# Kernel tuning notes

Hardware: AMD Instinct MI355X
Metric: run time of the kernel (lower is better)

## Reference

```python
import jax, jax.numpy as jnp
import numpy as np

N_CLASS = 20
N_SIGMA = 2
H = W = 512
B = 4
N_INST = 32
W_INST, W_VAR, W_SEED = 1.0, 10.0, 1.0
FG_WEIGHT = 10.0


def _xym():
    # channel 0: x along width, channel 1: y along height (matches torch buffer)
    xm = jnp.broadcast_to(jnp.linspace(0.0, 1.0, W)[None, :], (H, W))
    ym = jnp.broadcast_to(jnp.linspace(0.0, 1.0, H)[:, None], (H, W))
    return jnp.stack([xm, ym], axis=0)  # [2, H, W]


def lovasz_hinge_flat(logits, gt, valid):
    # logits, gt (0/1 float), valid (bool), all flat [P]; ignored pixels excluded
    P = logits.shape[0]
    vf = valid.astype(logits.dtype)
    signs = 2.0 * gt - 1.0
    # push ignored pixels to the end of the descending sort; relu(-1e9)=0 kills them
    errors = jnp.where(valid, 1.0 - logits * signs, -1e9)
    errors_sorted, perm = jax.lax.top_k(errors, P)  # descending
    gt_sorted = jnp.take(gt * vf, perm)
    v_sorted = jnp.take(vf, perm)
    gts = jnp.sum(gt * vf)
    inter = gts - jnp.cumsum(gt_sorted)
    union = gts + jnp.cumsum((1.0 - gt_sorted) * v_sorted)
    jac = 1.0 - inter / jnp.maximum(union, 1e-9)
    jac = jnp.concatenate([jac[:1], jac[1:] - jac[:-1]])
    return jnp.sum(jax.nn.relu(errors_sorted) * jac)


def _per_image(pred_b, inst_b, lab_b, xym, fg_w, n_inst):
    spatial_emb = jnp.tanh(pred_b[:2]) + xym            # [2,H,W]
    sigma = pred_b[2:2 + N_SIGMA]                       # [n_sigma,H,W]
    seed = jax.nn.sigmoid(pred_b[2 + N_SIGMA:2 + N_SIGMA + N_CLASS])  # [C,H,W]
    inst = inst_b[0]
    lab = lab_b[0]
    valid = (lab != 255)

    # background seed loss: sum over classes of seed^2 on pixels not of that class
    cls_ids = jnp.arange(N_CLASS)
    bg = (lab[None] != (cls_ids + 1)[:, None, None]) & valid[None]
    seed_bg = jnp.sum(jnp.square(seed) * bg)

    def per_inst(iid):
        m = (inst == iid)
        mf = m.astype(pred_b.dtype)
        cnt = jnp.maximum(jnp.sum(mf), 1.0)
        # to_center=True: center is mean coordinate of instance pixels
        center = jnp.sum(xym * mf[None], axis=(1, 2)) / cnt          # [2]
        s_mean = jnp.sum(sigma * mf[None], axis=(1, 2)) / cnt        # [n_sigma]
        var_l = jnp.sum(jnp.square(sigma - jax.lax.stop_gradient(s_mean)[:, None, None]) * mf[None]) / (N_SIGMA * cnt)
        s = jnp.exp(s_mean * 10.0)
        dist = jnp.exp(-jnp.sum(jnp.square(spatial_emb - center[:, None, None]) * s[:, None, None], axis=0))  # [H,W]
        inst_l = lovasz_hinge_flat((dist * 2.0 - 1.0).reshape(-1), mf.reshape(-1), valid.reshape(-1))
        cls = jnp.max(lab * m) - 1  # instance class (0-indexed)
        seed_c = jnp.take(seed, cls, axis=0)
        seed_fg = jnp.take(fg_w, cls) * jnp.sum(jnp.square(seed_c - jax.lax.stop_gradient(dist)) * mf)
        return inst_l, var_l, seed_fg

    inst_ls, var_ls, seed_fgs = jax.vmap(per_inst)(jnp.arange(1, n_inst + 1))
    instance_loss = jnp.sum(inst_ls) / n_inst
    var_loss = jnp.sum(var_ls) / n_inst
    seed_loss = (seed_bg + jnp.sum(seed_fgs)) / (H * W)
    return W_INST * instance_loss + W_VAR * var_loss + W_SEED * seed_loss


def setup_inputs() -> dict:
    key = jax.random.key(0)
    k1, k2 = jax.random.split(key)
    prediction = jax.random.normal(k1, (B, 2 + N_SIGMA + N_CLASS, H, W), dtype=jnp.float32)
    instances = jax.random.randint(k2, (B, 1, H, W), 0, N_INST + 1).astype(jnp.int32)
    # each instance id has a consistent class, as the torch instance_to_cls dict assumes
    labels = jnp.where(instances > 0, ((instances - 1) % N_CLASS) + 1, 0).astype(jnp.int32)
    return {"prediction": prediction, "instances": instances, "labels": labels, "n_instances": N_INST}


def reference(prediction, instances, labels, n_instances):
    xym = _xym()
    fg_w = jnp.full((N_CLASS,), FG_WEIGHT, dtype=prediction.dtype)
    per = jax.vmap(lambda p, i, l: _per_image(p, i, l, xym, fg_w, n_instances))(prediction, instances, labels)
    return jnp.mean(per) + jnp.sum(prediction) * 0.0
```

## Files before the change

### kernel.cpp

```cpp
#include <hip/hip_runtime.h>
#include <hip/hip_fp16.h>
#include <math.h>

#define HH 512
#define WW 512
#define BB 4
#define NCLS 20
#define NINST 32
#define NPIX (HH*WW)
#define NCH 24
#define NBIN 64
#define NCHUNK3 128
#define CPX3 2048
#define K3T 512
#define HSTR 33

#define OFF_PARTA  ((size_t)0)
#define OFF_PSEED  (OFF_PARTA + 2048*256*4)
#define OFF_STATS  (OFF_PSEED + 2048*8)
#define OFF_SEEDBG (OFF_STATS + 8*128*4)
#define OFF_VALID  (OFF_SEEDBG + 4*4)
#define OFF_SFG    (OFF_VALID + 4*4)
#define OFF_REC    ((OFF_SFG + 512*4 + 255) & ~(size_t)255)
#define OFF_HIST   (OFF_REC + (size_t)BB*NPIX*8)

__device__ __forceinline__ float fast_rcp(float x) { return __builtin_amdgcn_rcpf(x); }
__device__ __forceinline__ float fast_sigmoid(float z) { return fast_rcp(1.0f + __expf(-z)); }
__device__ __forceinline__ float fast_tanh(float x) {
  return 1.0f - 2.0f * fast_rcp(__expf(2.0f * x) + 1.0f);
}

__global__ __launch_bounds__(256) void k1_stats(
    const float* __restrict__ pred, const int* __restrict__ inst,
    const int* __restrict__ lab,
    float* __restrict__ partA, float2* __restrict__ partSeed,
    uint2* __restrict__ rec, float* __restrict__ outz)
{
  __shared__ unsigned s_st[4][NINST][9];
  __shared__ float s_seed, s_valid;
  int t = threadIdx.x;
  int w = t >> 6;
  for (int i = t; i < 4*NINST*9; i += 256) ((unsigned*)s_st)[i] = 0u;
  if (t == 0) { s_seed = 0.f; s_valid = 0.f; }
  if (blockIdx.x == 0 && t == 0) outz[0] = 0.f;
  __syncthreads();

  int b = blockIdx.x >> 9;
  int p = (blockIdx.x & 511) * 512 + t * 2;
  const float* pb = pred + (size_t)b*NCH*NPIX;
  float2 e0v = *(const float2*)(pb + p);
  float2 e1v = *(const float2*)(pb + NPIX + p);
  float2 g0v = *(const float2*)(pb + 2*NPIX + p);
  float2 g1v = *(const float2*)(pb + 3*NPIX + p);
  int2 idv = *(const int2*)(inst + (size_t)b*NPIX + p);
  int2 lbv = *(const int2*)(lab + (size_t)b*NPIX + p);

  #pragma unroll
  for (int u = 0; u < 2; ++u) {
    int px = p + u;
    int x = px & (WW-1);
    int y = px >> 9;
    float xm = x * (1.0f/(WW-1));
    float ym = y * (1.0f/(HH-1));
    float g0 = (&g0v.x)[u];
    float g1 = (&g1v.x)[u];
    int id = (&idv.x)[u];
    int lb = (&lbv.x)[u];
    if (id >= 1) {
      int j = id - 1;
      unsigned* row = s_st[w][j];
      atomicAdd(&row[0], 1u | ((lb != 255) ? 0x10000u : 0u));
      atomicAdd((float*)&row[1], xm);
      atomicAdd((float*)&row[2], ym);
      atomicAdd((float*)&row[3], g0);
      atomicAdd((float*)&row[4], g1);
      atomicAdd((float*)&row[5], g0*g0);
      atomicAdd((float*)&row[6], g1*g1);
    }
  }

  float so0 = 0.f, so1 = 0.f, Sv0 = 0.f, Sv1 = 0.f;
  #pragma unroll
  for (int g = 0; g < 4; ++g) {
    float2 svb[5];
    #pragma unroll
    for (int k = 0; k < 5; ++k)
      svb[k] = *(const float2*)(pb + (size_t)(4 + g*5 + k)*NPIX + p);
    #pragma unroll
    for (int k = 0; k < 5; ++k) {
      int c = g*5 + k;
      float sg0 = fast_sigmoid(svb[k].x);
      float sg1 = fast_sigmoid(svb[k].y);
      Sv0 += sg0*sg0;
      Sv1 += sg1*sg1;
      if (c + 1 == lbv.x) so0 = sg0;
      if (c + 1 == lbv.y) so1 = sg1;
    }
  }
  float seedloc = 0.f, vloc = 0.f;
  if (lbv.x != 255) { seedloc += Sv0 - so0*so0; vloc += 1.0f; }
  if (lbv.y != 255) { seedloc += Sv1 - so1*so1; vloc += 1.0f; }

  {
    uint2 r4[2];
    #pragma unroll
    for (int u = 0; u < 2; ++u) {
      int px = p + u;
      int x = px & (WW-1);
      int y = px >> 9;
      float ex = fast_tanh((&e0v.x)[u]) + x * (1.0f/(WW-1));
      float ey = fast_tanh((&e1v.x)[u]) + y * (1.0f/(HH-1));
      __half2 h = __floats2half2_rn(ex, ey);
      unsigned valid = (((&lbv.x)[u]) != 255) ? 1u : 0u;
      unsigned meta = (unsigned)(&idv.x)[u] | (valid << 7);
      float sou = u ? so1 : so0;
      r4[u].x = *reinterpret_cast<unsigned*>(&h);
      r4[u].y = (unsigned)(unsigned char)(sou*255.f + 0.5f) | (meta << 8);
    }
    *(uint4*)(rec + (size_t)b*NPIX + p) = make_uint4(r4[0].x, r4[0].y, r4[1].x, r4[1].y);
  }
  for (int o = 32; o; o >>= 1) {
    seedloc += __shfl_down(seedloc, o);
    vloc    += __shfl_down(vloc, o);
  }
  if ((t & 63) == 0) { atomicAdd(&s_seed, seedloc); atomicAdd(&s_valid, vloc); }
  __syncthreads();

  {
    int j = t & 31, f = t >> 5;
    float v;
    if (f == 0) {
      unsigned s = (s_st[0][j][0] & 0xFFFFu) + (s_st[1][j][0] & 0xFFFFu)
                 + (s_st[2][j][0] & 0xFFFFu) + (s_st[3][j][0] & 0xFFFFu);
      v = (float)s;
    } else if (f == 7) {
      unsigned s = (s_st[0][j][0] >> 16) + (s_st[1][j][0] >> 16)
                 + (s_st[2][j][0] >> 16) + (s_st[3][j][0] >> 16);
      v = (float)s;
    } else {
      v = __uint_as_float(s_st[0][j][f]) + __uint_as_float(s_st[1][j][f])
        + __uint_as_float(s_st[2][j][f]) + __uint_as_float(s_st[3][j][f]);
    }
    partA[(blockIdx.x << 8) + t] = v;
  }
  if (t == 0) partSeed[blockIdx.x] = make_float2(s_seed, s_valid);
}

__global__ __launch_bounds__(256) void k2a_reduce(
    const float* __restrict__ partA, const float2* __restrict__ partSeed,
    float* __restrict__ stats, float* __restrict__ seedbg,
    float* __restrict__ validT)
{
  int bid = blockIdx.x;
  int t = threadIdx.x;
  if (bid < 32) {
    __shared__ float red[256];
    int b = bid >> 3, f = bid & 7;
    int j = t & 31, grp = t >> 5;
    float s = 0.f;
    #pragma unroll 8
    for (int k = 0; k < 64; ++k)
      s += partA[((b*512 + grp*64 + k) << 8) + (f << 5) + j];
    red[t] = s; __syncthreads();
    for (int st = 128; st >= 32; st >>= 1) {
      if (t < st) red[t] += red[t + st];
      __syncthreads();
    }
    if (t < 32) stats[f*128 + b*32 + t] = red[t];
  } else {
    int img = t >> 6, slot = t & 63;
    float s = 0.f, v = 0.f;
    #pragma unroll
    for (int k = 0; k < 8; ++k) {
      float2 ps = partSeed[img*512 + slot*8 + k];
      s += ps.x; v += ps.y;
    }
    for (int o = 32; o; o >>= 1) {
      s += __shfl_down(s, o);
      v += __shfl_down(v, o);
    }
    if (slot == 0) { seedbg[img] = s; validT[img] = v; }
  }
}

__global__ __launch_bounds__(K3T) void k3_hist(
    const uint2* __restrict__ rec, const float* __restrict__ stats,
    unsigned* __restrict__ hist, float* __restrict__ sfg)
{
  __shared__ unsigned hc[NBIN*HSTR];
  __shared__ float sder[NINST][4];
  __shared__ float s_fg[8];
  int t = threadIdx.x;
  int bid = blockIdx.x;
  int b = bid >> 7;
  int chunk = bid & 127;
  for (int i = t; i < NBIN*HSTR; i += K3T) hc[i] = 0u;
  if (t < NINST) {
    int pr = b*NINST + t;
    float cnt = fmaxf(stats[0*128+pr], 1.0f);
    float rc = fast_rcp(cnt);
    sder[t][0] = stats[1*128+pr] * rc;
    sder[t][1] = stats[2*128+pr] * rc;
    sder[t][2] = -1.442695041f * __expf(10.f * stats[3*128+pr] * rc);
    sder[t][3] = -1.442695041f * __expf(10.f * stats[4*128+pr] * rc);
  }
  __syncthreads();

  int w = t >> 6, lane = t & 63;
  int j = lane & 31, jp1 = j + 1;
  float cx = sder[j][0], cy = sder[j][1];
  float s0 = sder[j][2], s1 = sder[j][3];
  const uint4* base4 = (const uint4*)(rec + (size_t)b*NPIX + chunk*CPX3)
                       + w*128 + (lane >> 5);
  unsigned* hrow = hc + j;
  float fg = 0.f;

  #pragma unroll 4
  for (int r = 0; r < 64; ++r) {
    uint4 rv = base4[r*2];
    #pragma unroll
    for (int u = 0; u < 2; ++u) {
      unsigned lo = u ? rv.z : rv.x;
      unsigned hi = u ? rv.w : rv.y;
      __half2 h;
      *reinterpret_cast<unsigned*>(&h) = lo;
      float2 e = __half22float2(h);
      float dx = e.x - cx, dy = e.y - cy;
      float dist = exp2f(dx*dx*s0 + dy*dy*s1);
      bool own = ((int)((hi >> 8) & 0x3F) == jp1);
      if (own) { float d = (float)(hi & 0xFFu)*(1.0f/255.f) - dist; fg += d*d; }
      if (hi & 0x8000u) {
        float f = own ? (1.0f - dist) : dist;
        unsigned bin = min((unsigned)(f * (float)NBIN), NBIN-1u);
        if (bin) atomicAdd(&hrow[bin*HSTR], own ? 0x10001u : 1u);
      }
    }
  }
  for (int o = 32; o; o >>= 1) fg += __shfl_down(fg, o);
  if (lane == 0) s_fg[w] = fg;
  __syncthreads();
  if (t == 0) {
    float s = 0.f;
    #pragma unroll
    for (int i = 0; i < 8; ++i) s += s_fg[i];
    sfg[bid] = 10.0f * s;
  }
  unsigned* out = hist + (size_t)(b*NCHUNK3 + chunk) * (NINST*NBIN);
  #pragma unroll
  for (int k = 0; k < NINST*NBIN/K3T; ++k) {
    int idx = k*K3T + t;
    out[idx] = hc[(idx & 63)*HSTR + (idx >> 6)];
  }
}

__global__ __launch_bounds__(512) void k4_final(
    const unsigned* __restrict__ hist, const float* __restrict__ stats,
    const float* __restrict__ validT, const float* __restrict__ seedbg,
    const float* __restrict__ sfg, float* __restrict__ out)
{
  __shared__ unsigned s_c[8][NBIN], s_p[8][NBIN];
  __shared__ unsigned rc[NBIN], rp[NBIN];
  __shared__ float s_L;
  int t = threadIdx.x;
  int pair = blockIdx.x;
  int b = pair >> 5, j = pair & 31;
  int grp = t >> 6, bin = t & 63;
  const unsigned* bp = hist + ((size_t)b*NCHUNK3*NINST + j)*NBIN + bin;
  unsigned c = 0, p = 0;
  #pragma unroll 8
  for (int ch = grp*16; ch < grp*16 + 16; ++ch) {
    unsigned v = bp[(size_t)ch * (NINST*NBIN)];
    c += v & 0xFFFFu; p += v >> 16;
  }
  s_c[grp][bin] = c; s_p[grp][bin] = p;
  __syncthreads();
  if (t < NBIN) {
    unsigned cc = 0, pp = 0;
    #pragma unroll
    for (int g = 0; g < 8; ++g) { cc += s_c[g][t]; pp += s_p[g][t]; }
    s_c[0][t] = cc; s_p[0][t] = pp;
    rc[t] = t ? cc : 0u; rp[t] = t ? pp : 0u;
  }
  __syncthreads();
  for (int st = 32; st; st >>= 1) {
    if (t < st) { rc[t] += rc[t+st]; rp[t] += rp[t+st]; }
    __syncthreads();
  }
  float G = stats[7*128+pair];
  if (t == 0) {
    s_c[0][0] = (unsigned)validT[b] - rc[0];
    s_p[0][0] = (unsigned)G - rp[0];
  }
  __syncthreads();

  if (t < 64) {
    int lane = t;
    int k = NBIN - 1 - lane;
    unsigned n = s_c[0][k], pp0 = s_p[0][k];
    for (int off = 1; off < 64; off <<= 1) {
      unsigned nn = __shfl_up(n, off);
      unsigned pq = __shfl_up(pp0, off);
      if (lane >= off) { n += nn; pp0 += pq; }
    }
    float fN = (float)n;
    float fP = (float)pp0;
    float uni = G + fN - fP;
    float J = 1.0f - (G - fP) / fmaxf(uni, 1e-9f);
    float Jp = __shfl_up(J, 1);
    if (lane == 0) Jp = 0.f;
    float v = (k + 0.5f) * (2.0f/NBIN);
    float L = v * (J - Jp);
    for (int o = 32; o; o >>= 1) L += __shfl_down(L, o);
    if (lane == 0) s_L = L;
  }
  __syncthreads();
  if (t == 0) {
    float cntA = stats[0*128+pair];
    float cnt = fmaxf(cntA, 1.0f);
    float s0 = stats[3*128+pair], s1 = stats[4*128+pair];
    float q0 = stats[5*128+pair], q1 = stats[6*128+pair];
    float sm0 = s0/cnt, sm1 = s1/cnt;
    float varnum = q0 - 2.f*sm0*s0 + cntA*sm0*sm0
                 + q1 - 2.f*sm1*s1 + cntA*sm1*sm1;
    float varl = varnum / (2.0f * cnt);
    atomicAdd(out, (s_L + 10.0f*varl) * (1.0f/(NINST*BB)));
  }
  if (pair == 0) {
    __shared__ float red[512];
    float acc = sfg[t];
    if (t < 4) acc += seedbg[t];
    red[t] = acc; __syncthreads();
    for (int st = 256; st; st >>= 1) {
      if (t < st) red[t] += red[t+st];
      __syncthreads();
    }
    if (t == 0) atomicAdd(out, red[0] * (1.0f/((float)NPIX*BB)));
  }
}

extern "C" void kernel_launch(void* const* d_in, const int* in_sizes, int n_in,
                              void* d_out, int out_size, void* d_ws, size_t ws_size,
                              hipStream_t stream)
{
  const float* pred = (const float*)d_in[0];
  const int* inst = (const int*)d_in[1];
  const int* lab  = (const int*)d_in[2];
  char* ws = (char*)d_ws;
  float* partA = (float*)(ws + OFF_PARTA);
  float2* partSeed = (float2*)(ws + OFF_PSEED);
  float* stats = (float*)(ws + OFF_STATS);
  float* seedbg = (float*)(ws + OFF_SEEDBG);
  float* validT = (float*)(ws + OFF_VALID);
  float* sfg = (float*)(ws + OFF_SFG);
  uint2* rec = (uint2*)(ws + OFF_REC);
  unsigned* hist = (unsigned*)(ws + OFF_HIST);

  hipLaunchKernelGGL(k1_stats, dim3(2048), dim3(256), 0, stream,
                     pred, inst, lab, partA, partSeed, rec, (float*)d_out);
  hipLaunchKernelGGL(k2a_reduce, dim3(33), dim3(256), 0, stream,
                     partA, partSeed, stats, seedbg, validT);
  hipLaunchKernelGGL(k3_hist, dim3(BB*NCHUNK3), dim3(K3T), 0, stream,
                     rec, stats, hist, sfg);
  hipLaunchKernelGGL(k4_final, dim3(128), dim3(512), 0, stream,
                     hist, stats, validT, seedbg, sfg, (float*)d_out);
}
```

Measured before the change: 87.49 us.

## Split seed-channel pass into separate per-class kernel with SoA byte records

Splits the first pass into a geometry/stats kernel and a separate seed kernel that processes one class channel per block, so the 20-channel sigmoid sweep runs with more parallelism and fully coalesced float4 reads. The packed 8-byte pixel record becomes separate arrays: half2 embeddings, a byte of id/valid meta, a byte of own-class seed, and a byte label that the seed kernel reads. This costs an extra kernel launch and extra workspace traffic for the byte arrays. sgown is written only on owning pixels, but it is read only where own is true, so stale bytes do no harm.

```diff
diff --git a/kernel.cpp b/kernel.cpp
--- a/kernel.cpp
+++ b/kernel.cpp
@@ -16,13 +16,17 @@
 #define HSTR 33
 
 #define OFF_PARTA  ((size_t)0)
-#define OFF_PSEED  (OFF_PARTA + 2048*256*4)
-#define OFF_STATS  (OFF_PSEED + 2048*8)
+#define OFF_PSEED  (OFF_PARTA + 1024*256*4)
+#define OFF_PARTV  (OFF_PSEED + 10240*4)
+#define OFF_STATS  (OFF_PARTV + 1024*4)
 #define OFF_SEEDBG (OFF_STATS + 8*128*4)
 #define OFF_VALID  (OFF_SEEDBG + 4*4)
 #define OFF_SFG    (OFF_VALID + 4*4)
-#define OFF_REC    ((OFF_SFG + 512*4 + 255) & ~(size_t)255)
-#define OFF_HIST   (OFF_REC + (size_t)BB*NPIX*8)
+#define OFF_RECXY  ((OFF_SFG + 512*4 + 255) & ~(size_t)255)
+#define OFF_META   (OFF_RECXY + (size_t)BB*NPIX*4)
+#define OFF_SGOWN  (OFF_META + (size_t)BB*NPIX)
+#define OFF_LAB8   (OFF_SGOWN + (size_t)BB*NPIX)
+#define OFF_HIST   (OFF_LAB8 + (size_t)BB*NPIX)
 
 __device__ __forceinline__ float fast_rcp(float x) { return __builtin_amdgcn_rcpf(x); }
 __device__ __forceinline__ float fast_sigmoid(float z) { return fast_rcp(1.0f + __expf(-z)); }
@@ -30,33 +34,35 @@
   return 1.0f - 2.0f * fast_rcp(__expf(2.0f * x) + 1.0f);
 }
 
-__global__ __launch_bounds__(256) void k1_stats(
+__global__ __launch_bounds__(256) void k0_geom(
     const float* __restrict__ pred, const int* __restrict__ inst,
     const int* __restrict__ lab,
-    float* __restrict__ partA, float2* __restrict__ partSeed,
-    uint2* __restrict__ rec, float* __restrict__ outz)
+    float* __restrict__ partA, float* __restrict__ partV,
+    unsigned* __restrict__ recxy, unsigned char* __restrict__ meta8,
+    unsigned char* __restrict__ lab8, float* __restrict__ outz)
 {
   __shared__ unsigned s_st[4][NINST][9];
-  __shared__ float s_seed, s_valid;
+  __shared__ float s_valid;
   int t = threadIdx.x;
   int w = t >> 6;
   for (int i = t; i < 4*NINST*9; i += 256) ((unsigned*)s_st)[i] = 0u;
-  if (t == 0) { s_seed = 0.f; s_valid = 0.f; }
+  if (t == 0) s_valid = 0.f;
   if (blockIdx.x == 0 && t == 0) outz[0] = 0.f;
   __syncthreads();
 
-  int b = blockIdx.x >> 9;
-  int p = (blockIdx.x & 511) * 512 + t * 2;
+  int b = blockIdx.x >> 8;
+  int p = (blockIdx.x & 255) * 1024 + t * 4;
   const float* pb = pred + (size_t)b*NCH*NPIX;
-  float2 e0v = *(const float2*)(pb + p);
-  float2 e1v = *(const float2*)(pb + NPIX + p);
-  float2 g0v = *(const float2*)(pb + 2*NPIX + p);
-  float2 g1v = *(const float2*)(pb + 3*NPIX + p);
-  int2 idv = *(const int2*)(inst + (size_t)b*NPIX + p);
-  int2 lbv = *(const int2*)(lab + (size_t)b*NPIX + p);
-
+  float4 e0v = *(const float4*)(pb + p);
+  float4 e1v = *(const float4*)(pb + NPIX + p);
+  float4 g0v = *(const float4*)(pb + 2*NPIX + p);
+  float4 g1v = *(const float4*)(pb + 3*NPIX + p);
+  int4 idv = *(const int4*)(inst + (size_t)b*NPIX + p);
+  int4 lbv = *(const int4*)(lab + (size_t)b*NPIX + p);
+
+  float vloc = 0.f;
   #pragma unroll
-  for (int u = 0; u < 2; ++u) {
+  for (int u = 0; u < 4; ++u) {
     int px = p + u;
     int x = px & (WW-1);
     int y = px >> 9;
@@ -66,6 +72,7 @@
     float g1 = (&g1v.x)[u];
     int id = (&idv.x)[u];
     int lb = (&lbv.x)[u];
+    if (lb != 255) vloc += 1.0f;
     if (id >= 1) {
       int j = id - 1;
       unsigned* row = s_st[w][j];
@@ -79,51 +86,28 @@
     }
   }
 
-  float so0 = 0.f, so1 = 0.f, Sv0 = 0.f, Sv1 = 0.f;
-  #pragma unroll
-  for (int g = 0; g < 4; ++g) {
-    float2 svb[5];
+  {
+    unsigned rx[4], mpk = 0, lpk = 0;
     #pragma unroll
-    for (int k = 0; k < 5; ++k)
-      svb[k] = *(const float2*)(pb + (size_t)(4 + g*5 + k)*NPIX + p);
-    #pragma unroll
-    for (int k = 0; k < 5; ++k) {
-      int c = g*5 + k;
-      float sg0 = fast_sigmoid(svb[k].x);
-      float sg1 = fast_sigmoid(svb[k].y);
-      Sv0 += sg0*sg0;
-      Sv1 += sg1*sg1;
-      if (c + 1 == lbv.x) so0 = sg0;
-      if (c + 1 == lbv.y) so1 = sg1;
-    }
-  }
-  float seedloc = 0.f, vloc = 0.f;
-  if (lbv.x != 255) { seedloc += Sv0 - so0*so0; vloc += 1.0f; }
-  if (lbv.y != 255) { seedloc += Sv1 - so1*so1; vloc += 1.0f; }
-
-  {
-    uint2 r4[2];
-    #pragma unroll
-    for (int u = 0; u < 2; ++u) {
+    for (int u = 0; u < 4; ++u) {
       int px = p + u;
       int x = px & (WW-1);
       int y = px >> 9;
       float ex = fast_tanh((&e0v.x)[u]) + x * (1.0f/(WW-1));
       float ey = fast_tanh((&e1v.x)[u]) + y * (1.0f/(HH-1));
       __half2 h = __floats2half2_rn(ex, ey);
-      unsigned valid = (((&lbv.x)[u]) != 255) ? 1u : 0u;
-      unsigned meta = (unsigned)(&idv.x)[u] | (valid << 7);
-      float sou = u ? so1 : so0;
-      r4[u].x = *reinterpret_cast<unsigned*>(&h);
-      r4[u].y = (unsigned)(unsigned char)(sou*255.f + 0.5f) | (meta << 8);
-    }
-    *(uint4*)(rec + (size_t)b*NPIX + p) = make_uint4(r4[0].x, r4[0].y, r4[1].x, r4[1].y);
-  }
-  for (int o = 32; o; o >>= 1) {
-    seedloc += __shfl_down(seedloc, o);
-    vloc    += __shfl_down(vloc, o);
-  }
-  if ((t & 63) == 0) { atomicAdd(&s_seed, seedloc); atomicAdd(&s_valid, vloc); }
+      rx[u] = *reinterpret_cast<unsigned*>(&h);
+      int lb = (&lbv.x)[u];
+      unsigned valid = (lb != 255) ? 1u : 0u;
+      mpk |= ((unsigned)((&idv.x)[u]) | (valid << 7)) << (8*u);
+      lpk |= ((unsigned)(unsigned char)lb) << (8*u);
+    }
+    *(uint4*)(recxy + (size_t)b*NPIX + p) = make_uint4(rx[0], rx[1], rx[2], rx[3]);
+    *(unsigned*)(meta8 + (size_t)b*NPIX + p) = mpk;
+    *(unsigned*)(lab8 + (size_t)b*NPIX + p) = lpk;
+  }
+  for (int o = 32; o; o >>= 1) vloc += __shfl_down(vloc, o);
+  if ((t & 63) == 0) atomicAdd(&s_valid, vloc);
   __syncthreads();
 
   {
@@ -143,11 +127,46 @@
     }
     partA[(blockIdx.x << 8) + t] = v;
   }
-  if (t == 0) partSeed[blockIdx.x] = make_float2(s_seed, s_valid);
+  if (t == 0) partV[blockIdx.x] = s_valid;
+}
+
+__global__ __launch_bounds__(256) void k1_seed(
+    const float* __restrict__ pred, const unsigned char* __restrict__ lab8,
+    float* __restrict__ partSeed, unsigned char* __restrict__ sgown)
+{
+  __shared__ float s_seed;
+  int t = threadIdx.x;
+  if (t == 0) s_seed = 0.f;
+  __syncthreads();
+  int b = blockIdx.y;
+  int c = blockIdx.x >> 7;
+  int chunk = blockIdx.x & 127;
+  int base = chunk*2048 + t*8;
+  const float* ch = pred + ((size_t)b*NCH + 4 + c)*NPIX;
+  float4 v0 = *(const float4*)(ch + base);
+  float4 v1 = *(const float4*)(ch + base + 4);
+  uint2 lb2 = *(const uint2*)(lab8 + (size_t)b*NPIX + base);
+  unsigned cp1 = (unsigned)(c + 1);
+
+  float local = 0.f;
+  #pragma unroll
+  for (int k = 0; k < 8; ++k) {
+    float z = (k < 4) ? (&v0.x)[k] : (&v1.x)[k-4];
+    unsigned lb = ((k < 4 ? lb2.x : lb2.y) >> (8*(k & 3))) & 0xFFu;
+    float sg = fast_sigmoid(z);
+    bool own = (lb == cp1);
+    if (lb != 255u && !own) local += sg*sg;
+    if (own) sgown[(size_t)b*NPIX + base + k] = (unsigned char)(sg*255.f + 0.5f);
+  }
+  for (int o = 32; o; o >>= 1) local += __shfl_down(local, o);
+  if ((t & 63) == 0) atomicAdd(&s_seed, local);
+  __syncthreads();
+  if (t == 0) partSeed[(b*20 + c)*128 + chunk] = s_seed;
 }
 
 __global__ __launch_bounds__(256) void k2a_reduce(
-    const float* __restrict__ partA, const float2* __restrict__ partSeed,
+    const float* __restrict__ partA, const float* __restrict__ partSeed,
+    const float* __restrict__ partV,
     float* __restrict__ stats, float* __restrict__ seedbg,
     float* __restrict__ validT)
 {
@@ -159,8 +178,8 @@
     int j = t & 31, grp = t >> 5;
     float s = 0.f;
     #pragma unroll 8
-    for (int k = 0; k < 64; ++k)
-      s += partA[((b*512 + grp*64 + k) << 8) + (f << 5) + j];
+    for (int k = 0; k < 32; ++k)
+      s += partA[((b*256 + grp*32 + k) << 8) + (f << 5) + j];
     red[t] = s; __syncthreads();
     for (int st = 128; st >= 32; st >>= 1) {
       if (t < st) red[t] += red[t + st];
@@ -168,23 +187,25 @@
     }
     if (t < 32) stats[f*128 + b*32 + t] = red[t];
   } else {
-    int img = t >> 6, slot = t & 63;
+    int img = t >> 6, lane = t & 63;
     float s = 0.f, v = 0.f;
+    #pragma unroll 8
+    for (int k = 0; k < 40; ++k)
+      s += partSeed[img*2560 + lane*40 + k];
     #pragma unroll
-    for (int k = 0; k < 8; ++k) {
-      float2 ps = partSeed[img*512 + slot*8 + k];
-      s += ps.x; v += ps.y;
-    }
+    for (int k = 0; k < 4; ++k)
+      v += partV[img*256 + lane*4 + k];
     for (int o = 32; o; o >>= 1) {
       s += __shfl_down(s, o);
       v += __shfl_down(v, o);
     }
-    if (slot == 0) { seedbg[img] = s; validT[img] = v; }
+    if (lane == 0) { seedbg[img] = s; validT[img] = v; }
   }
 }
 
 __global__ __launch_bounds__(K3T) void k3_hist(
-    const uint2* __restrict__ rec, const float* __restrict__ stats,
+    const unsigned* __restrict__ recxy, const unsigned char* __restrict__ meta8,
+    const unsigned char* __restrict__ sgown, const float* __restrict__ stats,
     unsigned* __restrict__ hist, float* __restrict__ sfg)
 {
   __shared__ unsigned hc[NBIN*HSTR];
@@ -210,26 +231,32 @@
   int j = lane & 31, jp1 = j + 1;
   float cx = sder[j][0], cy = sder[j][1];
   float s0 = sder[j][2], s1 = sder[j][3];
-  const uint4* base4 = (const uint4*)(rec + (size_t)b*NPIX + chunk*CPX3)
-                       + w*128 + (lane >> 5);
+  size_t cbase = (size_t)b*NPIX + chunk*CPX3;
+  int off = w*256 + ((lane >> 5) << 1);
   unsigned* hrow = hc + j;
   float fg = 0.f;
 
   #pragma unroll 4
   for (int r = 0; r < 64; ++r) {
-    uint4 rv = base4[r*2];
+    int p0 = off + r*4;
+    uint2 xy = *(const uint2*)(recxy + cbase + p0);
+    unsigned short mm = *(const unsigned short*)(meta8 + cbase + p0);
+    unsigned short ss = *(const unsigned short*)(sgown + cbase + p0);
     #pragma unroll
     for (int u = 0; u < 2; ++u) {
-      unsigned lo = u ? rv.z : rv.x;
-      unsigned hi = u ? rv.w : rv.y;
+      unsigned lo = u ? xy.y : xy.x;
+      unsigned meta = (mm >> (8*u)) & 0xFFu;
       __half2 h;
       *reinterpret_cast<unsigned*>(&h) = lo;
       float2 e = __half22float2(h);
       float dx = e.x - cx, dy = e.y - cy;
       float dist = exp2f(dx*dx*s0 + dy*dy*s1);
-      bool own = ((int)((hi >> 8) & 0x3F) == jp1);
-      if (own) { float d = (float)(hi & 0xFFu)*(1.0f/255.f) - dist; fg += d*d; }
-      if (hi & 0x8000u) {
+      bool own = ((int)(meta & 0x3Fu) == jp1);
+      if (own) {
+        float sg = (float)((ss >> (8*u)) & 0xFFu) * (1.0f/255.f);
+        float d = sg - dist; fg += d*d;
+      }
+      if (meta & 0x80u) {
         float f = own ? (1.0f - dist) : dist;
         unsigned bin = min((unsigned)(f * (float)NBIN), NBIN-1u);
         if (bin) atomicAdd(&hrow[bin*HSTR], own ? 0x10001u : 1u);
@@ -347,20 +374,27 @@
   const int* lab  = (const int*)d_in[2];
   char* ws = (char*)d_ws;
   float* partA = (float*)(ws + OFF_PARTA);
-  float2* partSeed = (float2*)(ws + OFF_PSEED);
+  float* partSeed = (float*)(ws + OFF_PSEED);
+  float* partV = (float*)(ws + OFF_PARTV);
   float* stats = (float*)(ws + OFF_STATS);
   float* seedbg = (float*)(ws + OFF_SEEDBG);
   float* validT = (float*)(ws + OFF_VALID);
   float* sfg = (float*)(ws + OFF_SFG);
-  uint2* rec = (uint2*)(ws + OFF_REC);
+  unsigned* recxy = (unsigned*)(ws + OFF_RECXY);
+  unsigned char* meta8 = (unsigned char*)(ws + OFF_META);
+  unsigned char* sgown = (unsigned char*)(ws + OFF_SGOWN);
+  unsigned char* lab8 = (unsigned char*)(ws + OFF_LAB8);
   unsigned* hist = (unsigned*)(ws + OFF_HIST);
 
-  hipLaunchKernelGGL(k1_stats, dim3(2048), dim3(256), 0, stream,
-                     pred, inst, lab, partA, partSeed, rec, (float*)d_out);
+  hipLaunchKernelGGL(k0_geom, dim3(1024), dim3(256), 0, stream,
+                     pred, inst, lab, partA, partV, recxy, meta8, lab8,
+                     (float*)d_out);
+  hipLaunchKernelGGL(k1_seed, dim3(20*128, BB), dim3(256), 0, stream,
+                     pred, lab8, partSeed, sgown);
   hipLaunchKernelGGL(k2a_reduce, dim3(33), dim3(256), 0, stream,
-                     partA, partSeed, stats, seedbg, validT);
+                     partA, partSeed, partV, stats, seedbg, validT);
   hipLaunchKernelGGL(k3_hist, dim3(BB*NCHUNK3), dim3(K3T), 0, stream,
-                     rec, stats, hist, sfg);
+                     recxy, meta8, sgown, stats, hist, sfg);
   hipLaunchKernelGGL(k4_final, dim3(128), dim3(512), 0, stream,
                      hist, stats, validT, seedbg, sfg, (float*)d_out);
 }
```

Result: slower. 98.22 us (+12.3%).
